# Kernel optimization log

Hardware: AMD Instinct MI355X
Metric: run time of the kernel (lower is better)

## Reference

```python
import jax, jax.numpy as jnp
import numpy as np

N_NODES = 100000
N_EDGES = 1600000
N_GRAPHS = 512
HIDDEN = 128
N_LAYERS = 3


def setup_inputs() -> dict:
    key = jax.random.key(0)
    ks = jax.random.split(key, 16)
    X = jax.random.normal(ks[0], (N_NODES, HIDDEN), dtype=jnp.float32)
    edge_index = jax.random.randint(ks[1], (2, N_EDGES), 0, N_NODES, dtype=jnp.int64)
    batch = jnp.sort(jax.random.randint(ks[2], (N_NODES,), 0, N_GRAPHS, dtype=jnp.int64))
    s = 1.0 / np.sqrt(HIDDEN)
    mlp_w1 = jax.random.normal(ks[3], (N_LAYERS, HIDDEN, HIDDEN), dtype=jnp.float32) * s
    mlp_b1 = jnp.zeros((N_LAYERS, HIDDEN), dtype=jnp.float32)
    mlp_w2 = jax.random.normal(ks[4], (N_LAYERS, HIDDEN, HIDDEN), dtype=jnp.float32) * s
    mlp_b2 = jnp.zeros((N_LAYERS, HIDDEN), dtype=jnp.float32)
    cls_w1 = jax.random.normal(ks[5], (HIDDEN * N_LAYERS, HIDDEN), dtype=jnp.float32) / np.sqrt(HIDDEN * N_LAYERS)
    cls_b1 = jnp.zeros((HIDDEN,), dtype=jnp.float32)
    cls_w2 = jax.random.normal(ks[6], (HIDDEN, HIDDEN), dtype=jnp.float32) * s
    cls_b2 = jnp.zeros((HIDDEN,), dtype=jnp.float32)
    cls_w3 = jax.random.normal(ks[7], (HIDDEN, 1), dtype=jnp.float32) * s
    cls_b3 = jnp.zeros((1,), dtype=jnp.float32)
    return {"X": X, "edge_index": edge_index, "batch": batch,
            "mlp_w1": mlp_w1, "mlp_b1": mlp_b1, "mlp_w2": mlp_w2, "mlp_b2": mlp_b2,
            "cls_w1": cls_w1, "cls_b1": cls_b1, "cls_w2": cls_w2, "cls_b2": cls_b2,
            "cls_w3": cls_w3, "cls_b3": cls_b3}


def reference(X, edge_index, batch, mlp_w1, mlp_b1, mlp_w2, mlp_b2,
              cls_w1, cls_b1, cls_w2, cls_b2, cls_w3, cls_b3):
    src, dst = edge_index[0], edge_index[1]
    xs = []
    for l in range(N_LAYERS):
        # GIN aggregation: sum_{j in N(i)} x_j ; eps = 0 so add self feature
        agg = jax.ops.segment_sum(X[src], dst, num_segments=N_NODES)  # [N, H]
        z = X + agg
        # 2-layer MLP update
        h = jax.nn.relu(z @ mlp_w1[l] + mlp_b1[l])
        h = h @ mlp_w2[l] + mlp_b2[l]
        # dropout is identity in eval; then relu
        X = jax.nn.relu(h)
        # global sum pooling per graph
        xs.append(jax.ops.segment_sum(X, batch, num_segments=N_GRAPHS))  # [G, H]
    h = jnp.concatenate(xs, axis=-1)  # JK 'cat' -> [G, H*L]
    h = jax.nn.relu(h @ cls_w1 + cls_b1)
    h = jax.nn.relu(h @ cls_w2 + cls_b2)
    logits = h @ cls_w3 + cls_b3  # [G, 1]
    return logits
```

## Files before the change

kernel.cpp:

```cpp
#include <hip/hip_runtime.h>
#include <hip/hip_fp16.h>
#include <cstddef>
#include <cstdint>

#define N_NODES   100000
#define N_EDGES   1600000
#define N_GRAPHS  512
#define HIDDEN    128
#define N_LAYERS  3

#define N_WIN        400
#define WIN_NODES    (N_NODES / N_WIN)
#define PLACE_BLOCKS 128
#define PCHUNK       (N_EDGES / PLACE_BLOCKS)

#define F2H_BLOCKS   ((N_NODES * HIDDEN / 8) / 256)
#define WCONV_BLOCKS (N_LAYERS * 2 * 16)
#define PZERO_BLOCKS ((N_GRAPHS * HIDDEN * N_LAYERS) / 256)
#define PREP_BLOCKS  (F2H_BLOCKS + WCONV_BLOCKS + PZERO_BLOCKS)

typedef _Float16 half8  __attribute__((ext_vector_type(8)));
typedef _Float16 half4v __attribute__((ext_vector_type(4)));
typedef _Float16 half2v __attribute__((ext_vector_type(2)));
typedef float    float8 __attribute__((ext_vector_type(8)));
typedef float    floatx4 __attribute__((ext_vector_type(4)));
typedef float    floatx2 __attribute__((ext_vector_type(2)));

__global__ __launch_bounds__(256) void win_count_kernel(const int* __restrict__ dst,
                                                        int* __restrict__ counts) {
    __shared__ int cs[N_WIN];
    for (int i = threadIdx.x; i < N_WIN; i += 256) cs[i] = 0;
    __syncthreads();
    const int4* d4 = (const int4*)(dst + blockIdx.x * PCHUNK);
    for (int i = threadIdx.x; i < PCHUNK / 4; i += 256) {
        int4 d = d4[i];
        atomicAdd(&cs[d.x / WIN_NODES], 1);
        atomicAdd(&cs[d.y / WIN_NODES], 1);
        atomicAdd(&cs[d.z / WIN_NODES], 1);
        atomicAdd(&cs[d.w / WIN_NODES], 1);
    }
    __syncthreads();
    for (int i = threadIdx.x; i < N_WIN; i += 256)
        counts[blockIdx.x * N_WIN + i] = cs[i];
}

__global__ __launch_bounds__(128) void win_scan1_kernel(const int* __restrict__ counts,
                                                        int* __restrict__ offsets,
                                                        int* __restrict__ colsum) {
    __shared__ int tmp[128];
    const int w = blockIdx.x;
    const int t = threadIdx.x;
    tmp[t] = counts[t * N_WIN + w];
    __syncthreads();
#pragma unroll
    for (int off = 1; off < 128; off <<= 1) {
        int u = (t >= off) ? tmp[t - off] : 0;
        __syncthreads();
        tmp[t] += u;
        __syncthreads();
    }
    offsets[t * N_WIN + w] = (t == 0) ? 0 : tmp[t - 1];
    if (t == 127) colsum[w] = tmp[127];
}

__global__ __launch_bounds__(512) void win_place_kernel(const int* __restrict__ src,
                                                        const int* __restrict__ dst,
                                                        const int* __restrict__ offsets,
                                                        const int* __restrict__ colsum,
                                                        int2* __restrict__ wedge) {
    __shared__ int ws[512];
    __shared__ int off[N_WIN];
    const int t = threadIdx.x;
    ws[t] = (t < N_WIN) ? colsum[t] : 0;
    __syncthreads();
#pragma unroll
    for (int o = 1; o < 512; o <<= 1) {
        int u = (t >= o) ? ws[t - o] : 0;
        __syncthreads();
        ws[t] += u;
        __syncthreads();
    }
    if (t < N_WIN) off[t] = offsets[blockIdx.x * N_WIN + t] + ((t == 0) ? 0 : ws[t - 1]);
    __syncthreads();
    const int4* d4 = (const int4*)(dst + blockIdx.x * PCHUNK);
    const int4* s4 = (const int4*)(src + blockIdx.x * PCHUNK);
    for (int i = t; i < PCHUNK / 4; i += 512) {
        int4 d = d4[i];
        int4 s = s4[i];
        int p0 = atomicAdd(&off[d.x / WIN_NODES], 1); wedge[p0] = make_int2(d.x, s.x);
        int p1 = atomicAdd(&off[d.y / WIN_NODES], 1); wedge[p1] = make_int2(d.y, s.y);
        int p2 = atomicAdd(&off[d.z / WIN_NODES], 1); wedge[p2] = make_int2(d.z, s.z);
        int p3 = atomicAdd(&off[d.w / WIN_NODES], 1); wedge[p3] = make_int2(d.w, s.w);
    }
}

__global__ __launch_bounds__(512) void win_csr_kernel(const int2* __restrict__ wedge,
                                                      const int* __restrict__ colsum,
                                                      int* __restrict__ row_ptr,
                                                      int* __restrict__ csr_src) {
    __shared__ int ws[512];
    __shared__ int cnt[WIN_NODES];
    __shared__ int bb[2];
    const int w = blockIdx.x, n0 = w * WIN_NODES, t = threadIdx.x;
    ws[t] = (t < N_WIN) ? colsum[t] : 0;
    __syncthreads();
#pragma unroll
    for (int o = 1; o < 512; o <<= 1) {
        int u = (t >= o) ? ws[t - o] : 0;
        __syncthreads();
        ws[t] += u;
        __syncthreads();
    }
    if (t == 0) { bb[0] = (w > 0) ? ws[w - 1] : 0; bb[1] = ws[w]; }
    if (w == N_WIN - 1 && t == 0) row_ptr[N_NODES] = ws[N_WIN - 1];
    for (int i = t; i < WIN_NODES; i += 512) cnt[i] = 0;
    __syncthreads();
    const int b0 = bb[0], b1 = bb[1];
    for (int e = b0 + t; e < b1; e += 512)
        atomicAdd(&cnt[wedge[e].x - n0], 1);
    __syncthreads();
    ws[t] = (t < WIN_NODES) ? cnt[t] : 0;
    __syncthreads();
#pragma unroll
    for (int o = 1; o < 512; o <<= 1) {
        int u = (t >= o) ? ws[t - o] : 0;
        __syncthreads();
        ws[t] += u;
        __syncthreads();
    }
    const int excl = (t == 0) ? 0 : ws[t - 1];
    if (t < WIN_NODES) {
        row_ptr[n0 + t] = b0 + excl;
        cnt[t] = b0 + excl;
    }
    __syncthreads();
    for (int e = b0 + t; e < b1; e += 512) {
        int2 ed = wedge[e];
        int p = atomicAdd(&cnt[ed.x - n0], 1);
        csr_src[p] = ed.y;
    }
}

__global__ __launch_bounds__(256) void prep_kernel(const float* __restrict__ X,
                                                   __half* __restrict__ hA,
                                                   unsigned char* __restrict__ outq,
                                                   const float* __restrict__ w1,
                                                   const float* __restrict__ w2,
                                                   __half* __restrict__ wt1,
                                                   __half* __restrict__ wt2,
                                                   float* __restrict__ pooled) {
    __shared__ float tile[32][33];
    const int b = blockIdx.x;
    if (b < F2H_BLOCKS) {
        int t = b * 256 + threadIdx.x;
        const float4* in4 = (const float4*)X;
        float4 a = in4[t * 2 + 0];
        float4 c = in4[t * 2 + 1];
        __half2* o2 = (__half2*)hA;
        o2[t * 4 + 0] = __floats2half2_rn(a.x, a.y);
        o2[t * 4 + 1] = __floats2half2_rn(a.z, a.w);
        o2[t * 4 + 2] = __floats2half2_rn(c.x, c.y);
        o2[t * 4 + 3] = __floats2half2_rn(c.z, c.w);
        unsigned r0 = 0, r1 = 0;
        r0 = __builtin_amdgcn_cvt_pk_fp8_f32(a.x, a.y, r0, false);
        r0 = __builtin_amdgcn_cvt_pk_fp8_f32(a.z, a.w, r0, true);
        r1 = __builtin_amdgcn_cvt_pk_fp8_f32(c.x, c.y, r1, false);
        r1 = __builtin_amdgcn_cvt_pk_fp8_f32(c.z, c.w, r1, true);
        ((uint2*)outq)[t] = make_uint2(r0, r1);
    } else if (b < F2H_BLOCKS + WCONV_BLOCKS) {
        const int bb = b - F2H_BLOCKS;
        const int mat = bb & 1;
        const int tt = (bb >> 1) & 15;
        const int l  = bb >> 5;
        const int ti = (tt >> 2) * 32, tj = (tt & 3) * 32;
        const float* W = (mat ? w2 : w1) + (size_t)l * HIDDEN * HIDDEN;
        __half* WT = (mat ? wt2 : wt1) + (size_t)l * HIDDEN * HIDDEN;
        const int r = threadIdx.x >> 5;
        const int c = threadIdx.x & 31;
#pragma unroll
        for (int rr = 0; rr < 4; ++rr)
            tile[r + 8 * rr][c] = W[(size_t)(ti + r + 8 * rr) * HIDDEN + tj + c];
        __syncthreads();
#pragma unroll
        for (int rr = 0; rr < 4; ++rr)
            WT[(size_t)(tj + r + 8 * rr) * HIDDEN + ti + c] =
                __float2half(tile[c][r + 8 * rr]);
    } else {
        int idx = (b - F2H_BLOCKS - WCONV_BLOCKS) * 256 + threadIdx.x;
        pooled[idx] = 0.f;
    }
}

__device__ __forceinline__ void acc_fp8x16(float* acc, uint4 v) {
    floatx2 f;
    f = __builtin_amdgcn_cvt_pk_f32_fp8(v.x, false); acc[0] += f.x;  acc[1] += f.y;
    f = __builtin_amdgcn_cvt_pk_f32_fp8(v.x, true);  acc[2] += f.x;  acc[3] += f.y;
    f = __builtin_amdgcn_cvt_pk_f32_fp8(v.y, false); acc[4] += f.x;  acc[5] += f.y;
    f = __builtin_amdgcn_cvt_pk_f32_fp8(v.y, true);  acc[6] += f.x;  acc[7] += f.y;
    f = __builtin_amdgcn_cvt_pk_f32_fp8(v.z, false); acc[8] += f.x;  acc[9] += f.y;
    f = __builtin_amdgcn_cvt_pk_f32_fp8(v.z, true);  acc[10] += f.x; acc[11] += f.y;
    f = __builtin_amdgcn_cvt_pk_f32_fp8(v.w, false); acc[12] += f.x; acc[13] += f.y;
    f = __builtin_amdgcn_cvt_pk_f32_fp8(v.w, true);  acc[14] += f.x; acc[15] += f.y;
}

__global__ void gather_kernel(const unsigned char* __restrict__ Xq,
                              const __half* __restrict__ Xh,
                              __half* __restrict__ Zh,
                              const int* __restrict__ row_ptr,
                              const int* __restrict__ csr_src) {
    int wave = (blockIdx.x * blockDim.x + threadIdx.x) >> 6;
    int lane = threadIdx.x & 63;
    if (wave >= N_NODES) return;
    const int grp = lane >> 3;
    const int m   = lane & 7;
    const uint4* Q = (const uint4*)Xq;

    float acc[16];
#pragma unroll
    for (int j = 0; j < 16; ++j) acc[j] = 0.f;

    int k = row_ptr[wave];
    const int end = row_ptr[wave + 1];

    for (; k + 16 <= end; k += 16) {
        int n0 = csr_src[k + grp];
        int n1 = csr_src[k + 8 + grp];
        uint4 v0 = Q[(size_t)n0 * 8 + m];
        uint4 v1 = Q[(size_t)n1 * 8 + m];
        acc_fp8x16(acc, v0);
        acc_fp8x16(acc, v1);
    }
    if (k + 8 <= end) {
        int n0 = csr_src[k + grp];
        uint4 v0 = Q[(size_t)n0 * 8 + m];
        acc_fp8x16(acc, v0);
        k += 8;
    }
    int rem = end - k;
    if (grp < rem) {
        int n0 = csr_src[k + grp];
        uint4 v0 = Q[(size_t)n0 * 8 + m];
        acc_fp8x16(acc, v0);
    }

    half2v hh[8];
#pragma unroll
    for (int j = 0; j < 8; ++j) {
        hh[j][0] = (_Float16)acc[2 * j];
        hh[j][1] = (_Float16)acc[2 * j + 1];
    }
#pragma unroll
    for (int j = 0; j < 8; ++j) {
        int b = __shfl_xor(__builtin_bit_cast(int, hh[j]), 8);
        hh[j] = hh[j] + __builtin_bit_cast(half2v, b);
    }
#pragma unroll
    for (int j = 0; j < 8; ++j) {
        int b = __shfl_xor(__builtin_bit_cast(int, hh[j]), 16);
        hh[j] = hh[j] + __builtin_bit_cast(half2v, b);
    }
#pragma unroll
    for (int j = 0; j < 8; ++j) {
        int b = __shfl_xor(__builtin_bit_cast(int, hh[j]), 32);
        hh[j] = hh[j] + __builtin_bit_cast(half2v, b);
    }

    if (grp == 0) {
        const half2v* H2 = (const half2v*)(Xh + (size_t)wave * HIDDEN + 16 * m);
        half8 o0, o1;
#pragma unroll
        for (int j = 0; j < 4; ++j) {
            half2v s = hh[j] + H2[j];
            o0[2 * j] = s[0]; o0[2 * j + 1] = s[1];
        }
#pragma unroll
        for (int j = 0; j < 4; ++j) {
            half2v s = hh[4 + j] + H2[4 + j];
            o1[2 * j] = s[0]; o1[2 * j + 1] = s[1];
        }
        ((half8*)(Zh + (size_t)wave * HIDDEN + 16 * m))[0] = o0;
        ((half8*)(Zh + (size_t)wave * HIDDEN + 16 * m))[1] = o1;
    }
}

#define MM_BLOCKS 512
__global__ __launch_bounds__(256, 2) void mm_stage_kernel(const __half* __restrict__ A,
                                                          const __half* __restrict__ Wt,
                                                          const float* __restrict__ bias,
                                                          __half* __restrict__ C16) {
    const int gwave = (blockIdx.x * 256 + threadIdx.x) >> 6;
    const int lane  = threadIdx.x & 63;
    const int m = lane & 15;
    const int q = lane >> 4;
    const int nwaves = MM_BLOCKS * 4;
    const int NTILES = N_NODES / 16;

    half8 wf[8][4];
    float bl[8][4];
#pragma unroll
    for (int ct = 0; ct < 8; ++ct) {
        const half8* Wrow = (const half8*)(Wt + (size_t)(ct * 16 + m) * HIDDEN);
#pragma unroll
        for (int c = 0; c < 4; ++c) wf[ct][c] = Wrow[c * 4 + q];
#pragma unroll
        for (int r = 0; r < 4; ++r) bl[ct][r] = bias[ct * 16 + q * 4 + r];
    }

    for (int t = gwave; t < NTILES; t += nwaves) {
        const half8* Arow = (const half8*)(A + (size_t)(t * 16 + m) * HIDDEN);
        half8 a0 = Arow[q];
        half8 a1 = Arow[4 + q];
        half8 a2 = Arow[8 + q];
        half8 a3 = Arow[12 + q];
        __half* Cr = C16 + (size_t)(t * 16 + m) * HIDDEN + q * 4;
#pragma unroll
        for (int ct = 0; ct < 8; ++ct) {
            floatx4 acc = {0.f, 0.f, 0.f, 0.f};
            acc = __builtin_amdgcn_mfma_f32_16x16x32_f16(wf[ct][0], a0, acc, 0, 0, 0);
            acc = __builtin_amdgcn_mfma_f32_16x16x32_f16(wf[ct][1], a1, acc, 0, 0, 0);
            acc = __builtin_amdgcn_mfma_f32_16x16x32_f16(wf[ct][2], a2, acc, 0, 0, 0);
            acc = __builtin_amdgcn_mfma_f32_16x16x32_f16(wf[ct][3], a3, acc, 0, 0, 0);
            half4v o;
#pragma unroll
            for (int r = 0; r < 4; ++r)
                o[r] = (_Float16)fmaxf(acc[r] + bl[ct][r], 0.f);
            *(half4v*)(Cr + ct * 16) = o;
        }
    }
}

#define POOL_CHUNK 32
__global__ __launch_bounds__(64) void pool_kernel(const __half* __restrict__ Xh,
                                                  const int* __restrict__ batch,
                                                  float* __restrict__ pooled, int layer,
                                                  unsigned char* __restrict__ outq) {
    const int f2 = threadIdx.x;
    int start = blockIdx.x * POOL_CHUNK;
    int end = start + POOL_CHUNK;
    if (end > N_NODES) end = N_NODES;
    float ax = 0.f, ay = 0.f;
    int gcur = batch[start];
    for (int n = start; n < end; ++n) {
        int g = batch[n];
        if (g != gcur) {
            float* pd = &pooled[(size_t)gcur * (HIDDEN * N_LAYERS) + layer * HIDDEN + 2 * f2];
            atomicAdd(pd, ax);
            atomicAdd(pd + 1, ay);
            ax = 0.f; ay = 0.f;
            gcur = g;
        }
        __half2 v = ((const __half2*)(Xh + (size_t)n * HIDDEN))[f2];
        float2 fv = __half22float2(v);
        ax += fv.x; ay += fv.y;
        if (outq) {
            unsigned r = __builtin_amdgcn_cvt_pk_fp8_f32(fv.x, fv.y, 0, false);
            ((unsigned short*)(outq + (size_t)n * HIDDEN))[f2] = (unsigned short)(r & 0xffff);
        }
    }
    float* pd = &pooled[(size_t)gcur * (HIDDEN * N_LAYERS) + layer * HIDDEN + 2 * f2];
    atomicAdd(pd, ax);
    atomicAdd(pd + 1, ay);
}

__global__ __launch_bounds__(128) void cls_kernel(const float* __restrict__ pooled,
                                                  const float* __restrict__ w1,
                                                  const float* __restrict__ b1,
                                                  const float* __restrict__ w2,
                                                  const float* __restrict__ b2,
                                                  const float* __restrict__ w3,
                                                  const float* __restrict__ b3,
                                                  float* __restrict__ out) {
    __shared__ float hin[HIDDEN * N_LAYERS];
    __shared__ float h1[HIDDEN];
    __shared__ float red[HIDDEN];
    const int g = blockIdx.x;
    const int t = threadIdx.x;

    for (int i = t; i < HIDDEN * N_LAYERS; i += 128)
        hin[i] = pooled[(size_t)g * (HIDDEN * N_LAYERS) + i];
    __syncthreads();

    float s = 0.f;
    for (int k = 0; k < HIDDEN * N_LAYERS; ++k) s += hin[k] * w1[(size_t)k * HIDDEN + t];
    s = fmaxf(s + b1[t], 0.f);
    h1[t] = s;
    __syncthreads();

    float s2 = 0.f;
    for (int k = 0; k < HIDDEN; ++k) s2 += h1[k] * w2[(size_t)k * HIDDEN + t];
    s2 = fmaxf(s2 + b2[t], 0.f);

    red[t] = s2 * w3[t];
    __syncthreads();
    for (int off = 64; off > 0; off >>= 1) {
        if (t < off) red[t] += red[t + off];
        __syncthreads();
    }
    if (t == 0) out[g] = red[0] + b3[0];
}

extern "C" void kernel_launch(void* const* d_in, const int* in_sizes, int n_in,
                              void* d_out, int out_size, void* d_ws, size_t ws_size,
                              hipStream_t stream) {
    const float* X     = (const float*)d_in[0];
    const int*   ei    = (const int*)d_in[1];
    const int*   batch = (const int*)d_in[2];
    const float* w1all = (const float*)d_in[3];
    const float* b1all = (const float*)d_in[4];
    const float* w2all = (const float*)d_in[5];
    const float* b2all = (const float*)d_in[6];
    const float* cw1   = (const float*)d_in[7];
    const float* cb1   = (const float*)d_in[8];
    const float* cw2   = (const float*)d_in[9];
    const float* cb2   = (const float*)d_in[10];
    const float* cw3   = (const float*)d_in[11];
    const float* cb3   = (const float*)d_in[12];
    float* out = (float*)d_out;

    const int* src = ei;
    const int* dst = ei + N_EDGES;

    char* p = (char*)d_ws;
    auto alloc2 = [&](size_t bytes) {
        char* r = p;
        p += (bytes + 255) & ~(size_t)255;
        return r;
    };
    __half* hA      = (__half*)alloc2((size_t)N_NODES * HIDDEN * sizeof(__half));
    __half* hB      = (__half*)alloc2((size_t)N_NODES * HIDDEN * sizeof(__half));
    __half* zh      = (__half*)alloc2((size_t)N_NODES * HIDDEN * sizeof(__half));
    __half* m1h     = (__half*)alloc2((size_t)N_NODES * HIDDEN * sizeof(__half));
    unsigned char* qbuf = (unsigned char*)alloc2((size_t)N_NODES * HIDDEN);
    __half* wt1     = (__half*)alloc2((size_t)N_LAYERS * HIDDEN * HIDDEN * sizeof(__half));
    __half* wt2     = (__half*)alloc2((size_t)N_LAYERS * HIDDEN * HIDDEN * sizeof(__half));
    int2*   wedge   = (int2*)alloc2((size_t)N_EDGES * sizeof(int2));
    int*    csr     = (int*)alloc2((size_t)N_EDGES * sizeof(int));
    int*    rowp    = (int*)alloc2((size_t)(N_NODES + 1) * sizeof(int));
    int*    counts  = (int*)alloc2((size_t)PLACE_BLOCKS * N_WIN * sizeof(int));
    int*    offsets = (int*)alloc2((size_t)PLACE_BLOCKS * N_WIN * sizeof(int));
    int*    colsum  = (int*)alloc2((size_t)N_WIN * sizeof(int));
    float*  pooled  = (float*)alloc2((size_t)N_GRAPHS * HIDDEN * N_LAYERS * sizeof(float));

    win_count_kernel<<<PLACE_BLOCKS, 256, 0, stream>>>(dst, counts);
    win_scan1_kernel<<<N_WIN, 128, 0, stream>>>(counts, offsets, colsum);
    win_place_kernel<<<PLACE_BLOCKS, 512, 0, stream>>>(src, dst, offsets, colsum, wedge);
    win_csr_kernel<<<N_WIN, 512, 0, stream>>>(wedge, colsum, rowp, csr);

    prep_kernel<<<PREP_BLOCKS, 256, 0, stream>>>(X, hA, qbuf, w1all, w2all, wt1, wt2, pooled);

    const int gat_grid  = (N_NODES + 3) / 4;
    const int pool_grid = (N_NODES + POOL_CHUNK - 1) / POOL_CHUNK;

    __half* hcur = hA;
    for (int l = 0; l < N_LAYERS; ++l) {
        __half* hnext = (l & 1) ? hA : hB;
        gather_kernel<<<gat_grid, 256, 0, stream>>>(qbuf, hcur, zh, rowp, csr);
        mm_stage_kernel<<<MM_BLOCKS, 256, 0, stream>>>(zh,
                                                       wt1 + (size_t)l * HIDDEN * HIDDEN,
                                                       b1all + (size_t)l * HIDDEN,
                                                       m1h);
        mm_stage_kernel<<<MM_BLOCKS, 256, 0, stream>>>(m1h,
                                                       wt2 + (size_t)l * HIDDEN * HIDDEN,
                                                       b2all + (size_t)l * HIDDEN,
                                                       hnext);
        pool_kernel<<<pool_grid, 64, 0, stream>>>(hnext, batch, pooled, l,
                                                  (l < N_LAYERS - 1) ? qbuf : nullptr);
        hcur = hnext;
    }

    cls_kernel<<<N_GRAPHS, 128, 0, stream>>>(pooled, cw1, cb1, cw2, cb2, cw3, cb3, out);
}
```

Before: 488.7 us.

## Fuse both MLP matmuls and graph pooling into one kernel per layer

Replaces the two mm_stage launches and the pool_kernel with a single kernel. The hidden activation of the first matmul stays in shared memory, and W2 is staged in LDS. The epilogue writes fp16 and fp8 node features, then does a wave-level shuffle reduction before atomic pooling into per-graph sums. This removes the m1h intermediate round trip, the re-read of the output for pooling, and two launches per layer. In exchange it adds LDS pressure, register pressure and more atomics when a tile spans graphs. It also skips writing features on the last layer.

```diff
diff --git a/kernel.cpp b/kernel.cpp
--- a/kernel.cpp
+++ b/kernel.cpp
@@ -283,28 +283,50 @@
     }
 }
 
-#define MM_BLOCKS 512
-__global__ __launch_bounds__(256, 2) void mm_stage_kernel(const __half* __restrict__ A,
-                                                          const __half* __restrict__ Wt,
-                                                          const float* __restrict__ bias,
-                                                          __half* __restrict__ C16) {
-    const int gwave = (blockIdx.x * 256 + threadIdx.x) >> 6;
-    const int lane  = threadIdx.x & 63;
-    const int m = lane & 15;
-    const int q = lane >> 4;
-    const int nwaves = MM_BLOCKS * 4;
+#define MLP_BLOCKS 512
+__global__ __launch_bounds__(256, 2) void mlp_fused_kernel(const __half* __restrict__ A,
+                                                           const __half* __restrict__ Wt1,
+                                                           const __half* __restrict__ Wt2,
+                                                           const float* __restrict__ b1,
+                                                           const float* __restrict__ b2,
+                                                           const int* __restrict__ batch,
+                                                           float* __restrict__ pooled,
+                                                           int layer,
+                                                           __half* __restrict__ H16,
+                                                           unsigned char* __restrict__ Q8) {
+    __shared__ __half w2s[128][136];
+    __shared__ float  bs[2][128];
+    __shared__ __half hs[4][16][136];
+
+    const int tid  = threadIdx.x;
+    const int wid  = tid >> 6;
+    const int lane = tid & 63;
+    const int m    = lane & 15;
+    const int q    = lane >> 4;
+
+    {
+        const half8* s8 = (const half8*)Wt2;
+        for (int j = tid; j < 128 * 16; j += 256) {
+            int r = j >> 4, c = j & 15;
+            *(half8*)&w2s[r][c * 8] = s8[j];
+        }
+        if (tid < 128) { bs[0][tid] = b1[tid]; bs[1][tid] = b2[tid]; }
+    }
+
+    half8 wf1[8][4];
+#pragma unroll
+    for (int ct = 0; ct < 8; ++ct) {
+        const half8* Wrow = (const half8*)(Wt1 + (size_t)(ct * 16 + m) * HIDDEN);
+#pragma unroll
+        for (int c = 0; c < 4; ++c) wf1[ct][c] = Wrow[c * 4 + q];
+    }
+    __syncthreads();
+
+    const int gwave  = (blockIdx.x * 256 + tid) >> 6;
+    const int nwaves = MLP_BLOCKS * 4;
     const int NTILES = N_NODES / 16;
 
-    half8 wf[8][4];
-    float bl[8][4];
-#pragma unroll
-    for (int ct = 0; ct < 8; ++ct) {
-        const half8* Wrow = (const half8*)(Wt + (size_t)(ct * 16 + m) * HIDDEN);
-#pragma unroll
-        for (int c = 0; c < 4; ++c) wf[ct][c] = Wrow[c * 4 + q];
-#pragma unroll
-        for (int r = 0; r < 4; ++r) bl[ct][r] = bias[ct * 16 + q * 4 + r];
-    }
+    _Float16* hrow = (_Float16*)&hs[wid][m][0];
 
     for (int t = gwave; t < NTILES; t += nwaves) {
         const half8* Arow = (const half8*)(A + (size_t)(t * 16 + m) * HIDDEN);
@@ -312,54 +334,86 @@
         half8 a1 = Arow[4 + q];
         half8 a2 = Arow[8 + q];
         half8 a3 = Arow[12 + q];
-        __half* Cr = C16 + (size_t)(t * 16 + m) * HIDDEN + q * 4;
+
 #pragma unroll
         for (int ct = 0; ct < 8; ++ct) {
             floatx4 acc = {0.f, 0.f, 0.f, 0.f};
-            acc = __builtin_amdgcn_mfma_f32_16x16x32_f16(wf[ct][0], a0, acc, 0, 0, 0);
-            acc = __builtin_amdgcn_mfma_f32_16x16x32_f16(wf[ct][1], a1, acc, 0, 0, 0);
-            acc = __builtin_amdgcn_mfma_f32_16x16x32_f16(wf[ct][2], a2, acc, 0, 0, 0);
-            acc = __builtin_amdgcn_mfma_f32_16x16x32_f16(wf[ct][3], a3, acc, 0, 0, 0);
+            acc = __builtin_amdgcn_mfma_f32_16x16x32_f16(wf1[ct][0], a0, acc, 0, 0, 0);
+            acc = __builtin_amdgcn_mfma_f32_16x16x32_f16(wf1[ct][1], a1, acc, 0, 0, 0);
+            acc = __builtin_amdgcn_mfma_f32_16x16x32_f16(wf1[ct][2], a2, acc, 0, 0, 0);
+            acc = __builtin_amdgcn_mfma_f32_16x16x32_f16(wf1[ct][3], a3, acc, 0, 0, 0);
+            const floatx4 bb = *(const floatx4*)&bs[0][ct * 16 + q * 4];
             half4v o;
 #pragma unroll
-            for (int r = 0; r < 4; ++r)
-                o[r] = (_Float16)fmaxf(acc[r] + bl[ct][r], 0.f);
-            *(half4v*)(Cr + ct * 16) = o;
+            for (int r = 0; r < 4; ++r) o[r] = (_Float16)fmaxf(acc[r] + bb[r], 0.f);
+            *(half4v*)(hrow + ct * 16 + q * 4) = o;
         }
-    }
-}
-
-#define POOL_CHUNK 32
-__global__ __launch_bounds__(64) void pool_kernel(const __half* __restrict__ Xh,
-                                                  const int* __restrict__ batch,
-                                                  float* __restrict__ pooled, int layer,
-                                                  unsigned char* __restrict__ outq) {
-    const int f2 = threadIdx.x;
-    int start = blockIdx.x * POOL_CHUNK;
-    int end = start + POOL_CHUNK;
-    if (end > N_NODES) end = N_NODES;
-    float ax = 0.f, ay = 0.f;
-    int gcur = batch[start];
-    for (int n = start; n < end; ++n) {
-        int g = batch[n];
-        if (g != gcur) {
-            float* pd = &pooled[(size_t)gcur * (HIDDEN * N_LAYERS) + layer * HIDDEN + 2 * f2];
-            atomicAdd(pd, ax);
-            atomicAdd(pd + 1, ay);
-            ax = 0.f; ay = 0.f;
-            gcur = g;
+        __builtin_amdgcn_sched_barrier(0);
+
+        half8 h0 = *(const half8*)(hrow + 8 * q);
+        half8 h1 = *(const half8*)(hrow + 32 + 8 * q);
+        half8 h2 = *(const half8*)(hrow + 64 + 8 * q);
+        half8 h3 = *(const half8*)(hrow + 96 + 8 * q);
+
+        const int g   = batch[t * 16 + m];
+        const int g0  = __shfl(g, 0);
+        const int g15 = __shfl(g, 15);
+        const bool uni = (g0 == g15);
+
+#pragma unroll
+        for (int ct = 0; ct < 8; ++ct) {
+            floatx4 facc = {0.f, 0.f, 0.f, 0.f};
+            const _Float16* w2row = (const _Float16*)&w2s[ct * 16 + m][0];
+            facc = __builtin_amdgcn_mfma_f32_16x16x32_f16(*(const half8*)(w2row + 8 * q),      h0, facc, 0, 0, 0);
+            facc = __builtin_amdgcn_mfma_f32_16x16x32_f16(*(const half8*)(w2row + 32 + 8 * q), h1, facc, 0, 0, 0);
+            facc = __builtin_amdgcn_mfma_f32_16x16x32_f16(*(const half8*)(w2row + 64 + 8 * q), h2, facc, 0, 0, 0);
+            facc = __builtin_amdgcn_mfma_f32_16x16x32_f16(*(const half8*)(w2row + 96 + 8 * q), h3, facc, 0, 0, 0);
+            const floatx4 b2v = *(const floatx4*)&bs[1][ct * 16 + q * 4];
+            float v0 = fmaxf(facc[0] + b2v[0], 0.f);
+            float v1 = fmaxf(facc[1] + b2v[1], 0.f);
+            float v2 = fmaxf(facc[2] + b2v[2], 0.f);
+            float v3 = fmaxf(facc[3] + b2v[3], 0.f);
+
+            const size_t base = (size_t)(t * 16 + m) * HIDDEN + ct * 16 + q * 4;
+            if (H16) {
+                half4v o;
+                o[0] = (_Float16)v0; o[1] = (_Float16)v1;
+                o[2] = (_Float16)v2; o[3] = (_Float16)v3;
+                *(half4v*)(H16 + base) = o;
+            }
+            if (Q8) {
+                unsigned r0 = 0;
+                r0 = __builtin_amdgcn_cvt_pk_fp8_f32(v0, v1, r0, false);
+                r0 = __builtin_amdgcn_cvt_pk_fp8_f32(v2, v3, r0, true);
+                *(unsigned*)(Q8 + base) = r0;
+            }
+
+            if (uni) {
+#pragma unroll
+                for (int msk = 1; msk < 16; msk <<= 1) {
+                    v0 += __shfl_xor(v0, msk);
+                    v1 += __shfl_xor(v1, msk);
+                    v2 += __shfl_xor(v2, msk);
+                    v3 += __shfl_xor(v3, msk);
+                }
+                if (m == 0) {
+                    float* pd = pooled + (size_t)g0 * (HIDDEN * N_LAYERS) +
+                                layer * HIDDEN + ct * 16 + q * 4;
+                    atomicAdd(pd + 0, v0);
+                    atomicAdd(pd + 1, v1);
+                    atomicAdd(pd + 2, v2);
+                    atomicAdd(pd + 3, v3);
+                }
+            } else {
+                float* pd = pooled + (size_t)g * (HIDDEN * N_LAYERS) +
+                            layer * HIDDEN + ct * 16 + q * 4;
+                atomicAdd(pd + 0, v0);
+                atomicAdd(pd + 1, v1);
+                atomicAdd(pd + 2, v2);
+                atomicAdd(pd + 3, v3);
+            }
         }
-        __half2 v = ((const __half2*)(Xh + (size_t)n * HIDDEN))[f2];
-        float2 fv = __half22float2(v);
-        ax += fv.x; ay += fv.y;
-        if (outq) {
-            unsigned r = __builtin_amdgcn_cvt_pk_fp8_f32(fv.x, fv.y, 0, false);
-            ((unsigned short*)(outq + (size_t)n * HIDDEN))[f2] = (unsigned short)(r & 0xffff);
-        }
-    }
-    float* pd = &pooled[(size_t)gcur * (HIDDEN * N_LAYERS) + layer * HIDDEN + 2 * f2];
-    atomicAdd(pd, ax);
-    atomicAdd(pd + 1, ay);
+    }
 }
 
 __global__ __launch_bounds__(128) void cls_kernel(const float* __restrict__ pooled,
@@ -429,7 +483,6 @@
     __half* hA      = (__half*)alloc2((size_t)N_NODES * HIDDEN * sizeof(__half));
     __half* hB      = (__half*)alloc2((size_t)N_NODES * HIDDEN * sizeof(__half));
     __half* zh      = (__half*)alloc2((size_t)N_NODES * HIDDEN * sizeof(__half));
-    __half* m1h     = (__half*)alloc2((size_t)N_NODES * HIDDEN * sizeof(__half));
     unsigned char* qbuf = (unsigned char*)alloc2((size_t)N_NODES * HIDDEN);
     __half* wt1     = (__half*)alloc2((size_t)N_LAYERS * HIDDEN * HIDDEN * sizeof(__half));
     __half* wt2     = (__half*)alloc2((size_t)N_LAYERS * HIDDEN * HIDDEN * sizeof(__half));
@@ -448,23 +501,21 @@
 
     prep_kernel<<<PREP_BLOCKS, 256, 0, stream>>>(X, hA, qbuf, w1all, w2all, wt1, wt2, pooled);
 
-    const int gat_grid  = (N_NODES + 3) / 4;
-    const int pool_grid = (N_NODES + POOL_CHUNK - 1) / POOL_CHUNK;
+    const int gat_grid = (N_NODES + 3) / 4;
 
     __half* hcur = hA;
     for (int l = 0; l < N_LAYERS; ++l) {
         __half* hnext = (l & 1) ? hA : hB;
+        const bool emit = (l < N_LAYERS - 1);
         gather_kernel<<<gat_grid, 256, 0, stream>>>(qbuf, hcur, zh, rowp, csr);
-        mm_stage_kernel<<<MM_BLOCKS, 256, 0, stream>>>(zh,
-                                                       wt1 + (size_t)l * HIDDEN * HIDDEN,
-                                                       b1all + (size_t)l * HIDDEN,
-                                                       m1h);
-        mm_stage_kernel<<<MM_BLOCKS, 256, 0, stream>>>(m1h,
-                                                       wt2 + (size_t)l * HIDDEN * HIDDEN,
-                                                       b2all + (size_t)l * HIDDEN,
-                                                       hnext);
-        pool_kernel<<<pool_grid, 64, 0, stream>>>(hnext, batch, pooled, l,
-                                                  (l < N_LAYERS - 1) ? qbuf : nullptr);
+        mlp_fused_kernel<<<MLP_BLOCKS, 256, 0, stream>>>(zh,
+                                                         wt1 + (size_t)l * HIDDEN * HIDDEN,
+                                                         wt2 + (size_t)l * HIDDEN * HIDDEN,
+                                                         b1all + (size_t)l * HIDDEN,
+                                                         b2all + (size_t)l * HIDDEN,
+                                                         batch, pooled, l,
+                                                         emit ? hnext : (__half*)nullptr,
+                                                         emit ? qbuf : (unsigned char*)nullptr);
         hcur = hnext;
     }
 
```

New measurement: 749.9 us. +53.4%, slower.

## Fuse second MLP matmul with graph sum pooling and fp8 quantization

Applied to the files above, without the earlier changes.

Replaces the separate pool kernel with a fused epilogue in the second MLP matmul. Each 16-row tile computes ReLU outputs, writes fp16 and fp8 copies only when a later layer needs them, and adds into the per-graph pooled sums. When all rows of a tile belong to one graph it reduces across lanes before a single atomic, otherwise it issues per-row atomics. This removes one kernel launch per layer and a full reread of the hidden activations, and skips the fp16/fp8 writes on the last layer, at the cost of more atomics into pooled and more register pressure in the matmul.

```diff
diff --git a/kernel.cpp b/kernel.cpp
--- a/kernel.cpp
+++ b/kernel.cpp
@@ -329,37 +329,96 @@
     }
 }
 
-#define POOL_CHUNK 32
-__global__ __launch_bounds__(64) void pool_kernel(const __half* __restrict__ Xh,
-                                                  const int* __restrict__ batch,
-                                                  float* __restrict__ pooled, int layer,
-                                                  unsigned char* __restrict__ outq) {
-    const int f2 = threadIdx.x;
-    int start = blockIdx.x * POOL_CHUNK;
-    int end = start + POOL_CHUNK;
-    if (end > N_NODES) end = N_NODES;
-    float ax = 0.f, ay = 0.f;
-    int gcur = batch[start];
-    for (int n = start; n < end; ++n) {
-        int g = batch[n];
-        if (g != gcur) {
-            float* pd = &pooled[(size_t)gcur * (HIDDEN * N_LAYERS) + layer * HIDDEN + 2 * f2];
-            atomicAdd(pd, ax);
-            atomicAdd(pd + 1, ay);
-            ax = 0.f; ay = 0.f;
-            gcur = g;
+__global__ __launch_bounds__(256, 2) void mm_pool_kernel(const __half* __restrict__ A,
+                                                         const __half* __restrict__ Wt,
+                                                         const float* __restrict__ bias,
+                                                         const int* __restrict__ batch,
+                                                         float* __restrict__ pooled,
+                                                         int layer,
+                                                         __half* __restrict__ H16,
+                                                         unsigned char* __restrict__ Q8) {
+    const int gwave = (blockIdx.x * 256 + threadIdx.x) >> 6;
+    const int lane  = threadIdx.x & 63;
+    const int m = lane & 15;
+    const int q = lane >> 4;
+    const int nwaves = MM_BLOCKS * 4;
+    const int NTILES = N_NODES / 16;
+
+    half8 wf[8][4];
+    float bl[8][4];
+#pragma unroll
+    for (int ct = 0; ct < 8; ++ct) {
+        const half8* Wrow = (const half8*)(Wt + (size_t)(ct * 16 + m) * HIDDEN);
+#pragma unroll
+        for (int c = 0; c < 4; ++c) wf[ct][c] = Wrow[c * 4 + q];
+#pragma unroll
+        for (int r = 0; r < 4; ++r) bl[ct][r] = bias[ct * 16 + q * 4 + r];
+    }
+
+    for (int t = gwave; t < NTILES; t += nwaves) {
+        const half8* Arow = (const half8*)(A + (size_t)(t * 16 + m) * HIDDEN);
+        half8 a0 = Arow[q];
+        half8 a1 = Arow[4 + q];
+        half8 a2 = Arow[8 + q];
+        half8 a3 = Arow[12 + q];
+
+        const int g   = batch[t * 16 + m];
+        const int g0  = __shfl(g, 0);
+        const int g15 = __shfl(g, 15);
+        const bool uni = (g0 == g15);
+
+#pragma unroll
+        for (int ct = 0; ct < 8; ++ct) {
+            floatx4 acc = {0.f, 0.f, 0.f, 0.f};
+            acc = __builtin_amdgcn_mfma_f32_16x16x32_f16(wf[ct][0], a0, acc, 0, 0, 0);
+            acc = __builtin_amdgcn_mfma_f32_16x16x32_f16(wf[ct][1], a1, acc, 0, 0, 0);
+            acc = __builtin_amdgcn_mfma_f32_16x16x32_f16(wf[ct][2], a2, acc, 0, 0, 0);
+            acc = __builtin_amdgcn_mfma_f32_16x16x32_f16(wf[ct][3], a3, acc, 0, 0, 0);
+            float v0 = fmaxf(acc[0] + bl[ct][0], 0.f);
+            float v1 = fmaxf(acc[1] + bl[ct][1], 0.f);
+            float v2 = fmaxf(acc[2] + bl[ct][2], 0.f);
+            float v3 = fmaxf(acc[3] + bl[ct][3], 0.f);
+
+            const size_t base = (size_t)(t * 16 + m) * HIDDEN + ct * 16 + q * 4;
+            if (H16) {
+                half4v o;
+                o[0] = (_Float16)v0; o[1] = (_Float16)v1;
+                o[2] = (_Float16)v2; o[3] = (_Float16)v3;
+                *(half4v*)(H16 + base) = o;
+            }
+            if (Q8) {
+                unsigned r0 = 0;
+                r0 = __builtin_amdgcn_cvt_pk_fp8_f32(v0, v1, r0, false);
+                r0 = __builtin_amdgcn_cvt_pk_fp8_f32(v2, v3, r0, true);
+                *(unsigned*)(Q8 + base) = r0;
+            }
+
+            if (uni) {
+#pragma unroll
+                for (int msk = 1; msk < 16; msk <<= 1) {
+                    v0 += __shfl_xor(v0, msk);
+                    v1 += __shfl_xor(v1, msk);
+                    v2 += __shfl_xor(v2, msk);
+                    v3 += __shfl_xor(v3, msk);
+                }
+                if (m == 0) {
+                    float* pd = pooled + (size_t)g0 * (HIDDEN * N_LAYERS) +
+                                layer * HIDDEN + ct * 16 + q * 4;
+                    unsafeAtomicAdd(pd + 0, v0);
+                    unsafeAtomicAdd(pd + 1, v1);
+                    unsafeAtomicAdd(pd + 2, v2);
+                    unsafeAtomicAdd(pd + 3, v3);
+                }
+            } else {
+                float* pd = pooled + (size_t)g * (HIDDEN * N_LAYERS) +
+                            layer * HIDDEN + ct * 16 + q * 4;
+                unsafeAtomicAdd(pd + 0, v0);
+                unsafeAtomicAdd(pd + 1, v1);
+                unsafeAtomicAdd(pd + 2, v2);
+                unsafeAtomicAdd(pd + 3, v3);
+            }
         }
-        __half2 v = ((const __half2*)(Xh + (size_t)n * HIDDEN))[f2];
-        float2 fv = __half22float2(v);
-        ax += fv.x; ay += fv.y;
-        if (outq) {
-            unsigned r = __builtin_amdgcn_cvt_pk_fp8_f32(fv.x, fv.y, 0, false);
-            ((unsigned short*)(outq + (size_t)n * HIDDEN))[f2] = (unsigned short)(r & 0xffff);
-        }
-    }
-    float* pd = &pooled[(size_t)gcur * (HIDDEN * N_LAYERS) + layer * HIDDEN + 2 * f2];
-    atomicAdd(pd, ax);
-    atomicAdd(pd + 1, ay);
+    }
 }
 
 __global__ __launch_bounds__(128) void cls_kernel(const float* __restrict__ pooled,
@@ -448,23 +507,23 @@
 
     prep_kernel<<<PREP_BLOCKS, 256, 0, stream>>>(X, hA, qbuf, w1all, w2all, wt1, wt2, pooled);
 
-    const int gat_grid  = (N_NODES + 3) / 4;
-    const int pool_grid = (N_NODES + POOL_CHUNK - 1) / POOL_CHUNK;
+    const int gat_grid = (N_NODES + 3) / 4;
 
     __half* hcur = hA;
     for (int l = 0; l < N_LAYERS; ++l) {
         __half* hnext = (l & 1) ? hA : hB;
+        const bool emit = (l < N_LAYERS - 1);
         gather_kernel<<<gat_grid, 256, 0, stream>>>(qbuf, hcur, zh, rowp, csr);
         mm_stage_kernel<<<MM_BLOCKS, 256, 0, stream>>>(zh,
                                                        wt1 + (size_t)l * HIDDEN * HIDDEN,
                                                        b1all + (size_t)l * HIDDEN,
                                                        m1h);
-        mm_stage_kernel<<<MM_BLOCKS, 256, 0, stream>>>(m1h,
-                                                       wt2 + (size_t)l * HIDDEN * HIDDEN,
-                                                       b2all + (size_t)l * HIDDEN,
-                                                       hnext);
-        pool_kernel<<<pool_grid, 64, 0, stream>>>(hnext, batch, pooled, l,
-                                                  (l < N_LAYERS - 1) ? qbuf : nullptr);
+        mm_pool_kernel<<<MM_BLOCKS, 256, 0, stream>>>(m1h,
+                                                      wt2 + (size_t)l * HIDDEN * HIDDEN,
+                                                      b2all + (size_t)l * HIDDEN,
+                                                      batch, pooled, l,
+                                                      emit ? hnext : (__half*)nullptr,
+                                                      emit ? qbuf : (unsigned char*)nullptr);
         hcur = hnext;
     }
 
```

Result: slower. 820.3 us (+67.9%).

## Fuse FP8 quantization into second matmul and pool per-graph via segment bounds

Applied to the files above, without the earlier changes.

The fp8 copy of node features used by the next layer's gather is now written directly from the second MLP matmul epilogue instead of in the pooling kernel. Pooling is replaced by a one-block-per-graph kernel that uses graph start offsets, found by binary search over the sorted batch array in the prep kernel. This removes the atomic-based pooling pass, its pooled-buffer zeroing and its per-node batch reads, at the cost of extra scattered 4-byte stores in the matmul. Load balance in pooling now depends on graph size variance.

```diff
diff --git a/kernel.cpp b/kernel.cpp
--- a/kernel.cpp
+++ b/kernel.cpp
@@ -16,8 +16,8 @@
 
 #define F2H_BLOCKS   ((N_NODES * HIDDEN / 8) / 256)
 #define WCONV_BLOCKS (N_LAYERS * 2 * 16)
-#define PZERO_BLOCKS ((N_GRAPHS * HIDDEN * N_LAYERS) / 256)
-#define PREP_BLOCKS  (F2H_BLOCKS + WCONV_BLOCKS + PZERO_BLOCKS)
+#define GB_BLOCKS    2
+#define PREP_BLOCKS  (F2H_BLOCKS + WCONV_BLOCKS + GB_BLOCKS)
 
 typedef _Float16 half8  __attribute__((ext_vector_type(8)));
 typedef _Float16 half4v __attribute__((ext_vector_type(4)));
@@ -148,7 +148,8 @@
                                                    const float* __restrict__ w2,
                                                    __half* __restrict__ wt1,
                                                    __half* __restrict__ wt2,
-                                                   float* __restrict__ pooled) {
+                                                   const int* __restrict__ batch,
+                                                   int* __restrict__ gstart) {
     __shared__ float tile[32][33];
     const int b = blockIdx.x;
     if (b < F2H_BLOCKS) {
@@ -186,8 +187,16 @@
             WT[(size_t)(tj + r + 8 * rr) * HIDDEN + ti + c] =
                 __float2half(tile[c][r + 8 * rr]);
     } else {
-        int idx = (b - F2H_BLOCKS - WCONV_BLOCKS) * 256 + threadIdx.x;
-        pooled[idx] = 0.f;
+        const int g = (b - F2H_BLOCKS - WCONV_BLOCKS) * 256 + threadIdx.x;
+        if (g < N_GRAPHS) {
+            int lo = 0, hi = N_NODES;
+            while (lo < hi) {
+                int mid = (lo + hi) >> 1;
+                if (batch[mid] < g) lo = mid + 1; else hi = mid;
+            }
+            gstart[g] = lo;
+        }
+        if (g == 0) gstart[N_GRAPHS] = N_NODES;
     }
 }
 
@@ -287,7 +296,8 @@
 __global__ __launch_bounds__(256, 2) void mm_stage_kernel(const __half* __restrict__ A,
                                                           const __half* __restrict__ Wt,
                                                           const float* __restrict__ bias,
-                                                          __half* __restrict__ C16) {
+                                                          __half* __restrict__ C16,
+                                                          unsigned char* __restrict__ Q8) {
     const int gwave = (blockIdx.x * 256 + threadIdx.x) >> 6;
     const int lane  = threadIdx.x & 63;
     const int m = lane & 15;
@@ -320,46 +330,54 @@
             acc = __builtin_amdgcn_mfma_f32_16x16x32_f16(wf[ct][1], a1, acc, 0, 0, 0);
             acc = __builtin_amdgcn_mfma_f32_16x16x32_f16(wf[ct][2], a2, acc, 0, 0, 0);
             acc = __builtin_amdgcn_mfma_f32_16x16x32_f16(wf[ct][3], a3, acc, 0, 0, 0);
+            float v0 = fmaxf(acc[0] + bl[ct][0], 0.f);
+            float v1 = fmaxf(acc[1] + bl[ct][1], 0.f);
+            float v2 = fmaxf(acc[2] + bl[ct][2], 0.f);
+            float v3 = fmaxf(acc[3] + bl[ct][3], 0.f);
             half4v o;
-#pragma unroll
-            for (int r = 0; r < 4; ++r)
-                o[r] = (_Float16)fmaxf(acc[r] + bl[ct][r], 0.f);
+            o[0] = (_Float16)v0; o[1] = (_Float16)v1;
+            o[2] = (_Float16)v2; o[3] = (_Float16)v3;
             *(half4v*)(Cr + ct * 16) = o;
+            if (Q8) {
+                unsigned r0 = 0;
+                r0 = __builtin_amdgcn_cvt_pk_fp8_f32(v0, v1, r0, false);
+                r0 = __builtin_amdgcn_cvt_pk_fp8_f32(v2, v3, r0, true);
+                *(unsigned*)(Q8 + (size_t)(t * 16 + m) * HIDDEN + ct * 16 + q * 4) = r0;
+            }
         }
     }
 }
 
-#define POOL_CHUNK 32
-__global__ __launch_bounds__(64) void pool_kernel(const __half* __restrict__ Xh,
-                                                  const int* __restrict__ batch,
-                                                  float* __restrict__ pooled, int layer,
-                                                  unsigned char* __restrict__ outq) {
-    const int f2 = threadIdx.x;
-    int start = blockIdx.x * POOL_CHUNK;
-    int end = start + POOL_CHUNK;
-    if (end > N_NODES) end = N_NODES;
-    float ax = 0.f, ay = 0.f;
-    int gcur = batch[start];
-    for (int n = start; n < end; ++n) {
-        int g = batch[n];
-        if (g != gcur) {
-            float* pd = &pooled[(size_t)gcur * (HIDDEN * N_LAYERS) + layer * HIDDEN + 2 * f2];
-            atomicAdd(pd, ax);
-            atomicAdd(pd + 1, ay);
-            ax = 0.f; ay = 0.f;
-            gcur = g;
-        }
-        __half2 v = ((const __half2*)(Xh + (size_t)n * HIDDEN))[f2];
-        float2 fv = __half22float2(v);
-        ax += fv.x; ay += fv.y;
-        if (outq) {
-            unsigned r = __builtin_amdgcn_cvt_pk_fp8_f32(fv.x, fv.y, 0, false);
-            ((unsigned short*)(outq + (size_t)n * HIDDEN))[f2] = (unsigned short)(r & 0xffff);
-        }
-    }
-    float* pd = &pooled[(size_t)gcur * (HIDDEN * N_LAYERS) + layer * HIDDEN + 2 * f2];
-    atomicAdd(pd, ax);
-    atomicAdd(pd + 1, ay);
+__global__ __launch_bounds__(256) void gpool_kernel(const __half* __restrict__ Xh,
+                                                    const int* __restrict__ gstart,
+                                                    float* __restrict__ pooled,
+                                                    int layer) {
+    __shared__ float red[16][16][8];
+    const int g  = blockIdx.x;
+    const int f8 = threadIdx.x & 15;
+    const int qt = threadIdx.x >> 4;
+    const int s = gstart[g], e = gstart[g + 1];
+
+    float acc[8];
+#pragma unroll
+    for (int j = 0; j < 8; ++j) acc[j] = 0.f;
+
+    for (int n = s + qt; n < e; n += 16) {
+        half8 v = ((const half8*)(Xh + (size_t)n * HIDDEN))[f8];
+#pragma unroll
+        for (int j = 0; j < 8; ++j) acc[j] += (float)v[j];
+    }
+#pragma unroll
+    for (int j = 0; j < 8; ++j) red[qt][f8][j] = acc[j];
+    __syncthreads();
+
+    if (threadIdx.x < 128) {
+        const int c = threadIdx.x;
+        float sum = 0.f;
+#pragma unroll
+        for (int p = 0; p < 16; ++p) sum += red[p][c >> 3][c & 7];
+        pooled[(size_t)g * (HIDDEN * N_LAYERS) + layer * HIDDEN + c] = sum;
+    }
 }
 
 __global__ __launch_bounds__(128) void cls_kernel(const float* __restrict__ pooled,
@@ -439,6 +457,7 @@
     int*    counts  = (int*)alloc2((size_t)PLACE_BLOCKS * N_WIN * sizeof(int));
     int*    offsets = (int*)alloc2((size_t)PLACE_BLOCKS * N_WIN * sizeof(int));
     int*    colsum  = (int*)alloc2((size_t)N_WIN * sizeof(int));
+    int*    gstart  = (int*)alloc2((size_t)(N_GRAPHS + 1) * sizeof(int));
     float*  pooled  = (float*)alloc2((size_t)N_GRAPHS * HIDDEN * N_LAYERS * sizeof(float));
 
     win_count_kernel<<<PLACE_BLOCKS, 256, 0, stream>>>(dst, counts);
@@ -446,25 +465,26 @@
     win_place_kernel<<<PLACE_BLOCKS, 512, 0, stream>>>(src, dst, offsets, colsum, wedge);
     win_csr_kernel<<<N_WIN, 512, 0, stream>>>(wedge, colsum, rowp, csr);
 
-    prep_kernel<<<PREP_BLOCKS, 256, 0, stream>>>(X, hA, qbuf, w1all, w2all, wt1, wt2, pooled);
-
-    const int gat_grid  = (N_NODES + 3) / 4;
-    const int pool_grid = (N_NODES + POOL_CHUNK - 1) / POOL_CHUNK;
+    prep_kernel<<<PREP_BLOCKS, 256, 0, stream>>>(X, hA, qbuf, w1all, w2all, wt1, wt2,
+                                                 batch, gstart);
+
+    const int gat_grid = (N_NODES + 3) / 4;
 
     __half* hcur = hA;
     for (int l = 0; l < N_LAYERS; ++l) {
         __half* hnext = (l & 1) ? hA : hB;
+        const bool emit = (l < N_LAYERS - 1);
         gather_kernel<<<gat_grid, 256, 0, stream>>>(qbuf, hcur, zh, rowp, csr);
         mm_stage_kernel<<<MM_BLOCKS, 256, 0, stream>>>(zh,
                                                        wt1 + (size_t)l * HIDDEN * HIDDEN,
                                                        b1all + (size_t)l * HIDDEN,
-                                                       m1h);
+                                                       m1h, (unsigned char*)nullptr);
         mm_stage_kernel<<<MM_BLOCKS, 256, 0, stream>>>(m1h,
                                                        wt2 + (size_t)l * HIDDEN * HIDDEN,
                                                        b2all + (size_t)l * HIDDEN,
-                                                       hnext);
-        pool_kernel<<<pool_grid, 64, 0, stream>>>(hnext, batch, pooled, l,
-                                                  (l < N_LAYERS - 1) ? qbuf : nullptr);
+                                                       hnext,
+                                                       emit ? qbuf : (unsigned char*)nullptr);
+        gpool_kernel<<<N_GRAPHS, 256, 0, stream>>>(hnext, gstart, pooled, l);
         hcur = hnext;
     }
 
```

After: 456.2 us. -6.6%, faster.
